# Kernel optimization log

Hardware: AMD Instinct MI355X
Metric: run time of the kernel (lower is better)

The kernel has to match this reference:

```python
import jax, jax.numpy as jnp
import numpy as np

SIGMA = 0.001
EPS_LOG = 1e-12
EPS_COS = 1e-8


def setup_inputs() -> dict:
    key = jax.random.key(0)
    k1, k2, k3, k4 = jax.random.split(key, 4)
    B, T, K, S, d = 32, 512, 8, 8, 300
    center_pos = jax.random.randint(k1, (B,), 0, T)
    query_token_ids = jax.random.randint(k2, (B, T), 0, 30000)
    center_sense_embeddings = jax.random.normal(k3, (B, K, d), dtype=jnp.float32)
    context_sense_embeddings = jax.random.normal(k4, (B, T - 1, S, d), dtype=jnp.float32)
    return {
        'center_pos': center_pos,
        'query_token_ids': query_token_ids,
        'center_sense_embeddings': center_sense_embeddings,
        'context_sense_embeddings': context_sense_embeddings,
    }


def reference(center_pos, query_token_ids, center_sense_embeddings, context_sense_embeddings):
    B, T = query_token_ids.shape
    d = center_sense_embeddings.shape[-1]
    # v: mean over senses of context tokens -> [B, C, d], C = T-1
    v = context_sense_embeddings.mean(axis=-2)
    # a: scaled dot between center senses and context vectors -> [B, C, K]
    a = jnp.einsum('bkd,bcd->bck', center_sense_embeddings, v) / jnp.sqrt(jnp.float32(d))
    # context positions: skip the center position (vectorized form of the per-batch loop)
    i = jnp.arange(T - 1)  # [C]
    ctx_pos = i[None, :] + (i[None, :] >= center_pos[:, None])  # [B, C]
    w = jnp.exp(-jnp.abs(ctx_pos - center_pos[:, None]).astype(jnp.float32) / SIGMA)
    logw = jnp.log(jnp.maximum(w, EPS_LOG))  # [B, C]
    alpha = jax.nn.softmax(a + logw[:, :, None], axis=1)  # softmax over context positions
    m = jnp.einsum('bck,bcd->bkd', alpha, v)  # [B, K, d]
    # cosine similarity along d (torch semantics: clamp each norm by eps)
    num = jnp.sum(center_sense_embeddings * m, axis=-1)
    n1 = jnp.linalg.norm(center_sense_embeddings, axis=-1)
    n2 = jnp.linalg.norm(m, axis=-1)
    s = num / (jnp.maximum(n1, EPS_COS) * jnp.maximum(n2, EPS_COS))  # [B, K]
    q = jax.nn.softmax(s, axis=-1)
    idx = jnp.argmax(q, axis=-1)  # [B]
    pooled = jnp.take_along_axis(center_sense_embeddings, idx[:, None, None], axis=1)[:, 0, :]  # [B, d]
    return pooled, q
```

## Files before the change

kernel.cpp:

```cpp
#include <hip/hip_runtime.h>

#define NB 32
#define NC 511
#define NK 8
#define NS 8
#define ND 300
#define ND4 75
#define NCHK 64
#define EPS_COS 1e-8f


__device__ __forceinline__ void f4add(float4& a, const float4& b) {
    a.x += b.x; a.y += b.y; a.z += b.z; a.w += b.w;
}

__global__ __launch_bounds__(512) void k_main(const float* __restrict__ ctx,
                                              const float* __restrict__ cen,
                                              float* __restrict__ part) {
    const int b     = blockIdx.x >> 6;
    const int chunk = blockIdx.x & 63;
    const int w     = threadIdx.x >> 6;
    const int lane  = threadIdx.x & 63;
    const int c     = chunk * 8 + w;
    const int i0 = lane;
    const int i1 = lane + 64;
    const bool has1 = (i1 < ND4);

    float4 acc0[NK] = {};
    float4 acc1[NK] = {};

    if (c < NC) {
        const float4* ctx4 = (const float4*)ctx + (size_t)(b * NC + c) * NS * ND4;
        const float4* cen4 = (const float4*)cen + (size_t)b * NK * ND4;

        float4 s0 = make_float4(0.f, 0.f, 0.f, 0.f);
        float4 s1 = make_float4(0.f, 0.f, 0.f, 0.f);
#pragma unroll
        for (int sj = 0; sj < NS; ++sj) {
            f4add(s0, ctx4[sj * ND4 + i0]);
            if (has1) f4add(s1, ctx4[sj * ND4 + i1]);
        }
        const float inv = 0.125f;
        s0.x *= inv; s0.y *= inv; s0.z *= inv; s0.w *= inv;
        s1.x *= inv; s1.y *= inv; s1.z *= inv; s1.w *= inv;

        float pk[NK];
#pragma unroll
        for (int k = 0; k < NK; ++k) {
            float4 ca = cen4[k * ND4 + i0];
            float p = ca.x * s0.x + ca.y * s0.y + ca.z * s0.z + ca.w * s0.w;
            if (has1) {
                float4 cb = cen4[k * ND4 + i1];
                p += cb.x * s1.x + cb.y * s1.y + cb.z * s1.z + cb.w * s1.w;
            }
            pk[k] = p;
        }
#pragma unroll
        for (int off = 32; off; off >>= 1) {
#pragma unroll
            for (int k = 0; k < NK; ++k) pk[k] += __shfl_xor(pk[k], off);
        }
        const float scale = 0.057735026919f;
#pragma unroll
        for (int k = 0; k < NK; ++k) {
            float wk = __expf(pk[k] * scale);
            acc0[k].x = wk * s0.x; acc0[k].y = wk * s0.y;
            acc0[k].z = wk * s0.z; acc0[k].w = wk * s0.w;
            acc1[k].x = wk * s1.x; acc1[k].y = wk * s1.y;
            acc1[k].z = wk * s1.z; acc1[k].w = wk * s1.w;
        }
    }

    __shared__ float4 slab[4 * NK * ND4];
#define SLAB_ST(slot) { float4* sp = slab + (slot) * NK * ND4;                  \
    _Pragma("unroll") for (int k = 0; k < NK; ++k) {                            \
        sp[k * ND4 + i0] = acc0[k];                                             \
        if (has1) sp[k * ND4 + i1] = acc1[k]; } }
#define SLAB_ADD(slot) { const float4* sp = slab + (slot) * NK * ND4;           \
    _Pragma("unroll") for (int k = 0; k < NK; ++k) {                            \
        f4add(acc0[k], sp[k * ND4 + i0]);                                       \
        if (has1) f4add(acc1[k], sp[k * ND4 + i1]); } }

    if (w >= 4) SLAB_ST(w - 4);
    __syncthreads();
    if (w < 4) SLAB_ADD(w);
    __syncthreads();
    if (w == 2 || w == 3) SLAB_ST(w - 2);
    __syncthreads();
    if (w < 2) SLAB_ADD(w);
    __syncthreads();
    if (w == 1) SLAB_ST(0);
    __syncthreads();
    if (w == 0) {
        SLAB_ADD(0);
        float4* pp = (float4*)part + (size_t)(b * NCHK + chunk) * NK * ND4;
#pragma unroll
        for (int k = 0; k < NK; ++k) {
            pp[k * ND4 + i0] = acc0[k];
            if (has1) pp[k * ND4 + i1] = acc1[k];
        }
    }
#undef SLAB_ST
#undef SLAB_ADD
}

__global__ __launch_bounds__(320) void k_red(const float* __restrict__ part,
                                             const float* __restrict__ cen,
                                             float* __restrict__ sv) {
    const int b = blockIdx.x >> 3;
    const int k = blockIdx.x & 7;
    const int t = threadIdx.x;
    const int lane = t & 63, w = t >> 6;

    float m = 0.f;
    float cv = 0.f;
    if (t < ND) {
        const float* p = part + ((size_t)b * NCHK * NK + k) * ND + t;
#pragma unroll 4
        for (int ch = 0; ch < NCHK; ++ch)
            m += p[(size_t)ch * NK * ND];
        cv = cen[(size_t)(b * NK + k) * ND + t];
    }
    float num = cv * m, n1 = cv * cv, n2 = m * m;
#pragma unroll
    for (int off = 32; off; off >>= 1) {
        num += __shfl_down(num, off);
        n1  += __shfl_down(n1, off);
        n2  += __shfl_down(n2, off);
    }
    __shared__ float red[5][3];
    if (lane == 0) { red[w][0] = num; red[w][1] = n1; red[w][2] = n2; }
    __syncthreads();
    if (t == 0) {
        float a0 = 0.f, a1 = 0.f, a2 = 0.f;
#pragma unroll
        for (int i = 0; i < 5; ++i) { a0 += red[i][0]; a1 += red[i][1]; a2 += red[i][2]; }
        float denom = fmaxf(sqrtf(a1), EPS_COS) * fmaxf(sqrtf(a2), EPS_COS);
        sv[b * NK + k] = a0 / denom;
    }
}

__global__ __launch_bounds__(256) void k_fin(const float* __restrict__ sv,
                                             const float* __restrict__ cen,
                                             float* __restrict__ out) {
    const int b = blockIdx.x;
    const int t = threadIdx.x;
    __shared__ int bidx;
    if (t == 0) {
        float s[NK];
#pragma unroll
        for (int k = 0; k < NK; ++k) s[k] = sv[b * NK + k];
        float mx = s[0];
#pragma unroll
        for (int k = 1; k < NK; ++k) mx = fmaxf(mx, s[k]);
        float e[NK], sum = 0.f;
#pragma unroll
        for (int k = 0; k < NK; ++k) { e[k] = __expf(s[k] - mx); sum += e[k]; }
        float inv = 1.f / sum;
        int best = 0; float bv = s[0];
#pragma unroll
        for (int k = 1; k < NK; ++k) if (s[k] > bv) { bv = s[k]; best = k; }
#pragma unroll
        for (int k = 0; k < NK; ++k)
            out[(size_t)NB * ND + b * NK + k] = e[k] * inv;
        bidx = best;
    }
    __syncthreads();
    const float* src = cen + (size_t)(b * NK + bidx) * ND;
    for (int idx = t; idx < ND; idx += 256)
        out[(size_t)b * ND + idx] = src[idx];
}

extern "C" void kernel_launch(void* const* d_in, const int* in_sizes, int n_in,
                              void* d_out, int out_size, void* d_ws, size_t ws_size,
                              hipStream_t stream) {
    const float* cen = (const float*)d_in[2];
    const float* ctx = (const float*)d_in[3];
    float* out = (float*)d_out;

    float* part = (float*)d_ws;
    float* sv   = part + (size_t)NB * NCHK * NK * ND;

    k_main<<<dim3(NB * NCHK), dim3(512), 0, stream>>>(ctx, cen, part);
    k_red<<<dim3(NB * NK), dim3(320), 0, stream>>>(part, cen, sv);
    k_fin<<<dim3(NB), dim3(256), 0, stream>>>(sv, cen, out);
}
```

Baseline: 274.8 us.

## Stage context tiles into LDS via async global_load_lds and loop tiles per block

Each block now handles 4 tiles of 8 context positions instead of one, and stages every tile into shared memory with direct global-to-LDS loads. Per-wave accumulators carry across tiles, so the partial buffer shrinks from 64 to 16 chunks per batch and the reduction kernel has less to sum. The aim is cheaper memory streaming and less partial-sum traffic. In exchange the grid has 512 blocks instead of 2048, the large LDS footprint limits occupancy, and loads are not overlapped with compute because each tile has a full barrier.

```diff
diff --git a/kernel.cpp b/kernel.cpp
--- a/kernel.cpp
+++ b/kernel.cpp
@@ -6,72 +6,98 @@
 #define NS 8
 #define ND 300
 #define ND4 75
-#define NCHK 64
+#define CPB 8
+#define NTILE 4
+#define NJ 16
+#define NCHK 16
 #define EPS_COS 1e-8f
+#define CTX_FLOATS ((size_t)NB * NC * NS * ND)
 
 
 __device__ __forceinline__ void f4add(float4& a, const float4& b) {
     a.x += b.x; a.y += b.y; a.z += b.z; a.w += b.w;
 }
 
-__global__ __launch_bounds__(512) void k_main(const float* __restrict__ ctx,
-                                              const float* __restrict__ cen,
-                                              float* __restrict__ part) {
-    const int b     = blockIdx.x >> 6;
-    const int chunk = blockIdx.x & 63;
-    const int w     = threadIdx.x >> 6;
-    const int lane  = threadIdx.x & 63;
-    const int c     = chunk * 8 + w;
+__global__ __launch_bounds__(512, 4) void k_main(const float* __restrict__ ctx,
+                                                 const float* __restrict__ cen,
+                                                 float* __restrict__ part) {
+    const int b    = blockIdx.x >> 4;
+    const int j    = blockIdx.x & 15;
+    const int w    = threadIdx.x >> 6;
+    const int lane = threadIdx.x & 63;
     const int i0 = lane;
     const int i1 = lane + 64;
     const bool has1 = (i1 < ND4);
 
+    __shared__ float4 sh4[4800];
+    float* sh = (float*)sh4;
+
     float4 acc0[NK] = {};
     float4 acc1[NK] = {};
-
-    if (c < NC) {
-        const float4* ctx4 = (const float4*)ctx + (size_t)(b * NC + c) * NS * ND4;
-        const float4* cen4 = (const float4*)cen + (size_t)b * NK * ND4;
-
-        float4 s0 = make_float4(0.f, 0.f, 0.f, 0.f);
-        float4 s1 = make_float4(0.f, 0.f, 0.f, 0.f);
-#pragma unroll
-        for (int sj = 0; sj < NS; ++sj) {
-            f4add(s0, ctx4[sj * ND4 + i0]);
-            if (has1) f4add(s1, ctx4[sj * ND4 + i1]);
+    const float4* cen4 = (const float4*)cen + (size_t)b * NK * ND4;
+    const float* gmax = ctx + CTX_FLOATS - 4;
+
+#pragma unroll 1
+    for (int t = 0; t < NTILE; ++t) {
+        const int c0 = (j * NTILE + t) * CPB;
+        const float* gbase = ctx + ((size_t)b * NC + c0) * (NS * ND);
+
+        for (int seg = w; seg < 75; seg += 8) {
+            const float* ga = gbase + seg * 256 + lane * 4;
+            if (ga > gmax) ga = gmax;
+            __builtin_amdgcn_global_load_lds(
+                (const __attribute__((address_space(1))) void*)ga,
+                (__attribute__((address_space(3))) void*)(sh + seg * 256),
+                16, 0, 0);
         }
-        const float inv = 0.125f;
-        s0.x *= inv; s0.y *= inv; s0.z *= inv; s0.w *= inv;
-        s1.x *= inv; s1.y *= inv; s1.z *= inv; s1.w *= inv;
-
-        float pk[NK];
-#pragma unroll
-        for (int k = 0; k < NK; ++k) {
-            float4 ca = cen4[k * ND4 + i0];
-            float p = ca.x * s0.x + ca.y * s0.y + ca.z * s0.z + ca.w * s0.w;
-            if (has1) {
-                float4 cb = cen4[k * ND4 + i1];
-                p += cb.x * s1.x + cb.y * s1.y + cb.z * s1.z + cb.w * s1.w;
-            }
-            pk[k] = p;
+        __syncthreads();
+
+        const int c = c0 + w;
+        if (c < NC) {
+            const float4* Lw = (const float4*)(sh + w * (NS * ND));
+            float4 s0 = make_float4(0.f, 0.f, 0.f, 0.f);
+            float4 s1 = make_float4(0.f, 0.f, 0.f, 0.f);
+#pragma unroll
+            for (int sj = 0; sj < NS; ++sj) {
+                f4add(s0, Lw[sj * ND4 + i0]);
+                if (has1) f4add(s1, Lw[sj * ND4 + i1]);
+            }
+            const float inv = 0.125f;
+            s0.x *= inv; s0.y *= inv; s0.z *= inv; s0.w *= inv;
+            s1.x *= inv; s1.y *= inv; s1.z *= inv; s1.w *= inv;
+
+            float pk[NK];
+#pragma unroll
+            for (int k = 0; k < NK; ++k) {
+                float4 ca = cen4[k * ND4 + i0];
+                float p = ca.x * s0.x + ca.y * s0.y + ca.z * s0.z + ca.w * s0.w;
+                if (has1) {
+                    float4 cb = cen4[k * ND4 + i1];
+                    p += cb.x * s1.x + cb.y * s1.y + cb.z * s1.z + cb.w * s1.w;
+                }
+                pk[k] = p;
+            }
+#pragma unroll
+            for (int off = 32; off; off >>= 1) {
+#pragma unroll
+                for (int k = 0; k < NK; ++k) pk[k] += __shfl_xor(pk[k], off);
+            }
+            const float scale = 0.057735026919f;
+#pragma unroll
+            for (int k = 0; k < NK; ++k) {
+                float wk = __expf(pk[k] * scale);
+                acc0[k].x += wk * s0.x; acc0[k].y += wk * s0.y;
+                acc0[k].z += wk * s0.z; acc0[k].w += wk * s0.w;
+                if (has1) {
+                    acc1[k].x += wk * s1.x; acc1[k].y += wk * s1.y;
+                    acc1[k].z += wk * s1.z; acc1[k].w += wk * s1.w;
+                }
+            }
         }
-#pragma unroll
-        for (int off = 32; off; off >>= 1) {
-#pragma unroll
-            for (int k = 0; k < NK; ++k) pk[k] += __shfl_xor(pk[k], off);
-        }
-        const float scale = 0.057735026919f;
-#pragma unroll
-        for (int k = 0; k < NK; ++k) {
-            float wk = __expf(pk[k] * scale);
-            acc0[k].x = wk * s0.x; acc0[k].y = wk * s0.y;
-            acc0[k].z = wk * s0.z; acc0[k].w = wk * s0.w;
-            acc1[k].x = wk * s1.x; acc1[k].y = wk * s1.y;
-            acc1[k].z = wk * s1.z; acc1[k].w = wk * s1.w;
-        }
-    }
-
-    __shared__ float4 slab[4 * NK * ND4];
+        __syncthreads();
+    }
+
+    float4* slab = sh4;
 #define SLAB_ST(slot) { float4* sp = slab + (slot) * NK * ND4;                  \
     _Pragma("unroll") for (int k = 0; k < NK; ++k) {                            \
         sp[k * ND4 + i0] = acc0[k];                                             \
@@ -93,7 +119,7 @@
     __syncthreads();
     if (w == 0) {
         SLAB_ADD(0);
-        float4* pp = (float4*)part + (size_t)(b * NCHK + chunk) * NK * ND4;
+        float4* pp = (float4*)part + (size_t)(b * NJ + j) * NK * ND4;
 #pragma unroll
         for (int k = 0; k < NK; ++k) {
             pp[k * ND4 + i0] = acc0[k];
@@ -115,8 +141,8 @@
     float m = 0.f;
     float cv = 0.f;
     if (t < ND) {
-        const float* p = part + ((size_t)b * NCHK * NK + k) * ND + t;
-#pragma unroll 4
+        const float* p = part + ((size_t)(b * NCHK) * NK + k) * ND + t;
+#pragma unroll
         for (int ch = 0; ch < NCHK; ++ch)
             m += p[(size_t)ch * NK * ND];
         cv = cen[(size_t)(b * NK + k) * ND + t];
@@ -181,7 +207,7 @@
     float* part = (float*)d_ws;
     float* sv   = part + (size_t)NB * NCHK * NK * ND;
 
-    k_main<<<dim3(NB * NCHK), dim3(512), 0, stream>>>(ctx, cen, part);
+    k_main<<<dim3(NB * NJ), dim3(512), 0, stream>>>(ctx, cen, part);
     k_red<<<dim3(NB * NK), dim3(320), 0, stream>>>(part, cen, sv);
     k_fin<<<dim3(NB), dim3(256), 0, stream>>>(sv, cen, out);
 }
```

Result: faster. 257.5 us (-6.3%).

## Process multiple contexts per wave with double-buffered nontemporal loads

Applied to the files above, without the earlier changes.

Each wave now handles eight context positions in sequence and accumulates them in registers. Loads for the next position are software-pipelined (register double-buffered) with the compute on the current one, and use nontemporal loads. The center embedding is held in registers, blocks shrink to 256 threads with fewer chunks per batch, and the partial buffer and reduction depth drop to 16. The aim is to keep more memory traffic in flight and cut shared-memory reduction and partial-sum overhead, at the cost of higher register pressure.

```diff
diff --git a/kernel.cpp b/kernel.cpp
--- a/kernel.cpp
+++ b/kernel.cpp
@@ -6,86 +6,117 @@
 #define NS 8
 #define ND 300
 #define ND4 75
-#define NCHK 64
+#define NJ 16
+#define CPW 8
+#define NCHK 16
 #define EPS_COS 1e-8f
 
 
-__device__ __forceinline__ void f4add(float4& a, const float4& b) {
-    a.x += b.x; a.y += b.y; a.z += b.z; a.w += b.w;
-}
-
-__global__ __launch_bounds__(512) void k_main(const float* __restrict__ ctx,
-                                              const float* __restrict__ cen,
-                                              float* __restrict__ part) {
-    const int b     = blockIdx.x >> 6;
-    const int chunk = blockIdx.x & 63;
-    const int w     = threadIdx.x >> 6;
-    const int lane  = threadIdx.x & 63;
-    const int c     = chunk * 8 + w;
+typedef float nfloat4 __attribute__((ext_vector_type(4)));
+
+__device__ __forceinline__ void n4add(nfloat4& a, const nfloat4& b) { a += b; }
+
+__device__ __forceinline__ void load_c(const float* __restrict__ ctx, int b, int c,
+                                       int i0, int i1, bool has1,
+                                       nfloat4* X, nfloat4* Y) {
+    const nfloat4* p = (const nfloat4*)ctx + (size_t)(b * NC + c) * (NS * ND4);
+#pragma unroll
+    for (int s = 0; s < NS; ++s)
+        X[s] = __builtin_nontemporal_load(&p[s * ND4 + i0]);
+    if (has1) {
+#pragma unroll
+        for (int s = 0; s < NS; ++s)
+            Y[s] = __builtin_nontemporal_load(&p[s * ND4 + i1]);
+    }
+}
+
+__device__ __forceinline__ void consume(nfloat4* X, nfloat4* Y,
+                                        const nfloat4* cenA,
+                                        const nfloat4* cen4,
+                                        int i0, int i1, bool has1, bool active,
+                                        nfloat4* acc0, nfloat4* acc1) {
+    n4add(X[0], X[1]); n4add(X[2], X[3]); n4add(X[4], X[5]); n4add(X[6], X[7]);
+    n4add(X[0], X[2]); n4add(X[4], X[6]);
+    n4add(X[0], X[4]);
+    n4add(Y[0], Y[1]); n4add(Y[2], Y[3]); n4add(Y[4], Y[5]); n4add(Y[6], Y[7]);
+    n4add(Y[0], Y[2]); n4add(Y[4], Y[6]);
+    n4add(Y[0], Y[4]);
+    const float inv = 0.125f;
+    nfloat4 s0 = X[0] * inv;
+    nfloat4 s1 = Y[0] * inv;
+
+    float pk[NK];
+#pragma unroll
+    for (int k = 0; k < NK; ++k) {
+        nfloat4 ca = cenA[k];
+        float p = ca.x * s0.x + ca.y * s0.y + ca.z * s0.z + ca.w * s0.w;
+        if (has1) {
+            nfloat4 cb = cen4[k * ND4 + i1];
+            p += cb.x * s1.x + cb.y * s1.y + cb.z * s1.z + cb.w * s1.w;
+        }
+        pk[k] = p;
+    }
+#pragma unroll
+    for (int off = 32; off; off >>= 1) {
+#pragma unroll
+        for (int k = 0; k < NK; ++k) pk[k] += __shfl_xor(pk[k], off);
+    }
+    if (active) {
+        const float scale = 0.057735026919f;
+#pragma unroll
+        for (int k = 0; k < NK; ++k) {
+            float wk = __expf(pk[k] * scale);
+            acc0[k] += wk * s0;
+            if (has1) acc1[k] += wk * s1;
+        }
+    }
+}
+
+__global__ __launch_bounds__(256, 2) void k_main(const float* __restrict__ ctx,
+                                                 const float* __restrict__ cen,
+                                                 float* __restrict__ part) {
+    const int b    = blockIdx.x >> 4;
+    const int j    = blockIdx.x & 15;
+    const int w    = threadIdx.x >> 6;
+    const int lane = threadIdx.x & 63;
     const int i0 = lane;
     const int i1 = lane + 64;
     const bool has1 = (i1 < ND4);
-
-    float4 acc0[NK] = {};
-    float4 acc1[NK] = {};
-
-    if (c < NC) {
-        const float4* ctx4 = (const float4*)ctx + (size_t)(b * NC + c) * NS * ND4;
-        const float4* cen4 = (const float4*)cen + (size_t)b * NK * ND4;
-
-        float4 s0 = make_float4(0.f, 0.f, 0.f, 0.f);
-        float4 s1 = make_float4(0.f, 0.f, 0.f, 0.f);
-#pragma unroll
-        for (int sj = 0; sj < NS; ++sj) {
-            f4add(s0, ctx4[sj * ND4 + i0]);
-            if (has1) f4add(s1, ctx4[sj * ND4 + i1]);
-        }
-        const float inv = 0.125f;
-        s0.x *= inv; s0.y *= inv; s0.z *= inv; s0.w *= inv;
-        s1.x *= inv; s1.y *= inv; s1.z *= inv; s1.w *= inv;
-
-        float pk[NK];
-#pragma unroll
-        for (int k = 0; k < NK; ++k) {
-            float4 ca = cen4[k * ND4 + i0];
-            float p = ca.x * s0.x + ca.y * s0.y + ca.z * s0.z + ca.w * s0.w;
-            if (has1) {
-                float4 cb = cen4[k * ND4 + i1];
-                p += cb.x * s1.x + cb.y * s1.y + cb.z * s1.z + cb.w * s1.w;
-            }
-            pk[k] = p;
-        }
-#pragma unroll
-        for (int off = 32; off; off >>= 1) {
-#pragma unroll
-            for (int k = 0; k < NK; ++k) pk[k] += __shfl_xor(pk[k], off);
-        }
-        const float scale = 0.057735026919f;
-#pragma unroll
-        for (int k = 0; k < NK; ++k) {
-            float wk = __expf(pk[k] * scale);
-            acc0[k].x = wk * s0.x; acc0[k].y = wk * s0.y;
-            acc0[k].z = wk * s0.z; acc0[k].w = wk * s0.w;
-            acc1[k].x = wk * s1.x; acc1[k].y = wk * s1.y;
-            acc1[k].z = wk * s1.z; acc1[k].w = wk * s1.w;
-        }
-    }
-
-    __shared__ float4 slab[4 * NK * ND4];
-#define SLAB_ST(slot) { float4* sp = slab + (slot) * NK * ND4;                  \
+    const int cbase = j * 32 + w * CPW;
+
+    const nfloat4* cen4 = (const nfloat4*)cen + (size_t)b * NK * ND4;
+    nfloat4 cenA[NK];
+#pragma unroll
+    for (int k = 0; k < NK; ++k) cenA[k] = cen4[k * ND4 + i0];
+
+    nfloat4 acc0[NK] = {};
+    nfloat4 acc1[NK] = {};
+    nfloat4 XA[NS], YA[NS] = {}, XB[NS], YB[NS] = {};
+
+    load_c(ctx, b, min(cbase, NC - 1), i0, i1, has1, XA, YA);
+#pragma unroll
+    for (int i = 0; i < CPW; ++i) {
+        const int c = cbase + i;
+        nfloat4* Xc = (i & 1) ? XB : XA;
+        nfloat4* Yc = (i & 1) ? YB : YA;
+        nfloat4* Xn = (i & 1) ? XA : XB;
+        nfloat4* Yn = (i & 1) ? YA : YB;
+        if (i + 1 < CPW)
+            load_c(ctx, b, min(c + 1, NC - 1), i0, i1, has1, Xn, Yn);
+        consume(Xc, Yc, cenA, cen4, i0, i1, has1, c < NC, acc0, acc1);
+    }
+
+    __shared__ nfloat4 slab[2 * NK * ND4];
+#define SLAB_ST(slot) { nfloat4* sp = slab + (slot) * NK * ND4;                 \
     _Pragma("unroll") for (int k = 0; k < NK; ++k) {                            \
         sp[k * ND4 + i0] = acc0[k];                                             \
         if (has1) sp[k * ND4 + i1] = acc1[k]; } }
-#define SLAB_ADD(slot) { const float4* sp = slab + (slot) * NK * ND4;           \
+#define SLAB_ADD(slot) { const nfloat4* sp = slab + (slot) * NK * ND4;          \
     _Pragma("unroll") for (int k = 0; k < NK; ++k) {                            \
-        f4add(acc0[k], sp[k * ND4 + i0]);                                       \
-        if (has1) f4add(acc1[k], sp[k * ND4 + i1]); } }
-
-    if (w >= 4) SLAB_ST(w - 4);
-    __syncthreads();
-    if (w < 4) SLAB_ADD(w);
-    __syncthreads();
-    if (w == 2 || w == 3) SLAB_ST(w - 2);
+        acc0[k] += sp[k * ND4 + i0];                                            \
+        if (has1) acc1[k] += sp[k * ND4 + i1]; } }
+
+    if (w >= 2) SLAB_ST(w - 2);
     __syncthreads();
     if (w < 2) SLAB_ADD(w);
     __syncthreads();
@@ -93,7 +124,7 @@
     __syncthreads();
     if (w == 0) {
         SLAB_ADD(0);
-        float4* pp = (float4*)part + (size_t)(b * NCHK + chunk) * NK * ND4;
+        nfloat4* pp = (nfloat4*)part + (size_t)(b * NJ + j) * NK * ND4;
 #pragma unroll
         for (int k = 0; k < NK; ++k) {
             pp[k * ND4 + i0] = acc0[k];
@@ -115,8 +146,8 @@
     float m = 0.f;
     float cv = 0.f;
     if (t < ND) {
-        const float* p = part + ((size_t)b * NCHK * NK + k) * ND + t;
-#pragma unroll 4
+        const float* p = part + ((size_t)(b * NCHK) * NK + k) * ND + t;
+#pragma unroll
         for (int ch = 0; ch < NCHK; ++ch)
             m += p[(size_t)ch * NK * ND];
         cv = cen[(size_t)(b * NK + k) * ND + t];
@@ -181,7 +212,7 @@
     float* part = (float*)d_ws;
     float* sv   = part + (size_t)NB * NCHK * NK * ND;
 
-    k_main<<<dim3(NB * NCHK), dim3(512), 0, stream>>>(ctx, cen, part);
+    k_main<<<dim3(NB * NJ), dim3(256), 0, stream>>>(ctx, cen, part);
     k_red<<<dim3(NB * NK), dim3(320), 0, stream>>>(part, cen, sv);
     k_fin<<<dim3(NB), dim3(256), 0, stream>>>(sv, cen, out);
 }
```

New measurement: 478.4 us. 1.74x slower.
